# Optimization experiments

Hardware: AMD Instinct MI355X
Metric: run time of the kernel (lower is better)

## Reference

```python
import jax, jax.numpy as jnp
import numpy as np

EPS = 1e-5  # haiku LayerNorm default
BIG = 1e9


def layernorm(x, scale, offset):
    mu = jnp.mean(x, axis=-1, keepdims=True)
    var = jnp.var(x, axis=-1, keepdims=True)
    return scale * (x - mu) * jax.lax.rsqrt(var + EPS) + offset


def setup_inputs() -> dict:
    key = jax.random.key(0)
    ks = iter(jax.random.split(key, 32))
    N_res, N_tok, C, H = 4096, 512, 384, 8
    kd = C // H  # 48, key_dim and value_dim per head
    F = 4 * C    # transition hidden
    s = 0.02
    inp = {
        "original": jax.random.normal(next(ks), (1, N_res, C), jnp.float32),
        "resampled": jax.random.normal(next(ks), (1, N_tok, C), jnp.float32),
        "attention_mask": (jax.random.uniform(next(ks), (H, N_tok, N_res)) < 0.9).astype(jnp.float32),
        "output_mask": jnp.ones((1, N_tok), jnp.float32),
        "input_mask": jnp.ones((1, N_res), jnp.float32),
        # cross-attention LayerNorms
        "qn_scale": jnp.ones((C,), jnp.float32), "qn_offset": jnp.zeros((C,), jnp.float32),
        "dn_scale": jnp.ones((C,), jnp.float32), "dn_offset": jnp.zeros((C,), jnp.float32),
        # attention projections
        "query_w": jax.random.normal(next(ks), (C, H, kd), jnp.float32) * s,
        "key_w": jax.random.normal(next(ks), (C, H, kd), jnp.float32) * s,
        "value_w": jax.random.normal(next(ks), (C, H, kd), jnp.float32) * s,
        "gating_w": jax.random.normal(next(ks), (C, H, kd), jnp.float32) * s,
        "gating_b": jnp.ones((H, kd), jnp.float32),
        "output_w": jax.random.normal(next(ks), (H, kd, C), jnp.float32) * s,
        "output_b": jnp.zeros((C,), jnp.float32),
        # resampled transition
        "rt_ln_scale": jnp.ones((C,), jnp.float32), "rt_ln_offset": jnp.zeros((C,), jnp.float32),
        "rt_w1": jax.random.normal(next(ks), (C, F), jnp.float32) * s, "rt_b1": jnp.zeros((F,), jnp.float32),
        "rt_w2": jax.random.normal(next(ks), (F, C), jnp.float32) * s, "rt_b2": jnp.zeros((C,), jnp.float32),
        # original transition
        "ot_ln_scale": jnp.ones((C,), jnp.float32), "ot_ln_offset": jnp.zeros((C,), jnp.float32),
        "ot_w1": jax.random.normal(next(ks), (C, F), jnp.float32) * s, "ot_b1": jnp.zeros((F,), jnp.float32),
        "ot_w2": jax.random.normal(next(ks), (F, C), jnp.float32) * s, "ot_b2": jnp.zeros((C,), jnp.float32),
    }
    return inp


def reference(original, resampled, attention_mask, output_mask, input_mask,
              qn_scale, qn_offset, dn_scale, dn_offset,
              query_w, key_w, value_w, gating_w, gating_b, output_w, output_b,
              rt_ln_scale, rt_ln_offset, rt_w1, rt_b1, rt_w2, rt_b2,
              ot_ln_scale, ot_ln_offset, ot_w1, ot_b1, ot_w2, ot_b2):
    # ---- CrossAttention (deterministic; dropout rate 0) ----
    bias = BIG * (attention_mask - 1.0)          # [H, T, R]
    q_in = layernorm(resampled, qn_scale, qn_offset)   # [1, T, C]
    d_in = layernorm(original, dn_scale, dn_offset)    # [1, R, C]
    kd = query_w.shape[-1]
    q = jnp.einsum('bqa,ahc->bqhc', q_in, query_w) * kd ** (-0.5)
    k = jnp.einsum('bka,ahc->bkhc', d_in, key_w)
    v = jnp.einsum('bka,ahc->bkhc', d_in, value_w)
    logits = jnp.einsum('bqhc,bkhc->bhqk', q, k) + bias[None]  # [1, H, T, R]
    weights = jax.nn.softmax(logits, axis=-1)
    weighted_avg = jnp.einsum('bhqk,bkhc->bqhc', weights, v)
    gate = jax.nn.sigmoid(jnp.einsum('bqc,chv->bqhv', q_in, gating_w) + gating_b)
    weighted_avg = weighted_avg * gate
    attn_out = jnp.einsum('bqhc,hco->bqo', weighted_avg, output_w) + output_b
    resampled = resampled + attn_out             # residual (dropout off)
    # ---- resampled Transition + residual ----
    t = layernorm(resampled, rt_ln_scale, rt_ln_offset)
    t = jax.nn.relu(t @ rt_w1 + rt_b1) @ rt_w2 + rt_b2
    resampled = resampled + t
    # ---- original Transition + residual ----
    t = layernorm(original, ot_ln_scale, ot_ln_offset)
    t = jax.nn.relu(t @ ot_w1 + ot_b1) @ ot_w2 + ot_b2
    original = original + t
    return resampled.astype(jnp.float32), original.astype(jnp.float32)
```

## Files before the change

kernel.cpp:

```cpp
#include <hip/hip_runtime.h>
#include <hip/hip_bf16.h>
#include <cstdint>

typedef unsigned short u16;
typedef __attribute__((ext_vector_type(8))) __bf16 bf16x8;
typedef __attribute__((ext_vector_type(4))) float f32x4;
typedef __attribute__((ext_vector_type(4))) short s16x4;

#define VSTR 4160

__device__ __forceinline__ u16 f2bf(float f) {
  union { float f; unsigned u; } v; v.f = f;
  unsigned r = (v.u + 0x7FFFu + ((v.u >> 16) & 1u)) >> 16;
  return (u16)r;
}

__device__ __forceinline__ void gll16(const u16* gp, u16* lp) {
  auto g1 = reinterpret_cast<const __attribute__((address_space(1))) void*>(
      reinterpret_cast<uintptr_t>(gp));
  auto l3 = reinterpret_cast<__attribute__((address_space(3))) void*>(
      reinterpret_cast<uintptr_t>(lp));
  __builtin_amdgcn_global_load_lds(g1, l3, 16, 0, 0);
}

__global__ __launch_bounds__(128) void ln_all(
    const float* __restrict__ orig, const float* __restrict__ resam,
    const float* __restrict__ dn_s, const float* __restrict__ dn_o, u16* __restrict__ dinb,
    const float* __restrict__ ot_s, const float* __restrict__ ot_o, u16* __restrict__ otin,
    const float* __restrict__ qn_s, const float* __restrict__ qn_o, u16* __restrict__ qin) {
  const int row = blockIdx.x;
  const int t = threadIdx.x;
  const bool isOrig = row < 4096;
  const float* xr = isOrig ? orig + (size_t)row * 384 : resam + (size_t)(row - 4096) * 384;
  float v0 = xr[t], v1 = xr[t + 128], v2 = xr[t + 256];
  float sum = v0 + v1 + v2;
  float sq = v0 * v0 + v1 * v1 + v2 * v2;
#pragma unroll
  for (int off = 32; off > 0; off >>= 1) {
    sum += __shfl_xor(sum, off);
    sq += __shfl_xor(sq, off);
  }
  __shared__ float red[4];
  if ((t & 63) == 0) { red[(t >> 6) * 2] = sum; red[(t >> 6) * 2 + 1] = sq; }
  __syncthreads();
  sum = red[0] + red[2];
  sq = red[1] + red[3];
  const float mu = sum * (1.f / 384.f);
  const float rstd = rsqrtf(sq * (1.f / 384.f) - mu * mu + 1e-5f);
#pragma unroll
  for (int j = 0; j < 3; ++j) {
    const int cc = t + 128 * j;
    const float xv = (j == 0 ? v0 : (j == 1 ? v1 : v2));
    const float xn = (xv - mu) * rstd;
    if (isOrig) {
      dinb[(size_t)row * 384 + cc] = f2bf(dn_s[cc] * xn + dn_o[cc]);
      otin[(size_t)row * 384 + cc] = f2bf(ot_s[cc] * xn + ot_o[cc]);
    } else {
      qin[(size_t)(row - 4096) * 384 + cc] = f2bf(qn_s[cc] * xn + qn_o[cc]);
    }
  }
}

__global__ __launch_bounds__(128) void ln_kernel(
    const float* __restrict__ x,
    const float* __restrict__ s1, const float* __restrict__ o1, u16* __restrict__ y1) {
  const int row = blockIdx.x;
  const int t = threadIdx.x;
  const float* xr = x + (size_t)row * 384;
  float v0 = xr[t], v1 = xr[t + 128], v2 = xr[t + 256];
  float sum = v0 + v1 + v2;
  float sq = v0 * v0 + v1 * v1 + v2 * v2;
#pragma unroll
  for (int off = 32; off > 0; off >>= 1) {
    sum += __shfl_xor(sum, off);
    sq += __shfl_xor(sq, off);
  }
  __shared__ float red[4];
  if ((t & 63) == 0) { red[(t >> 6) * 2] = sum; red[(t >> 6) * 2 + 1] = sq; }
  __syncthreads();
  sum = red[0] + red[2];
  sq = red[1] + red[3];
  const float mu = sum * (1.f / 384.f);
  const float rstd = rsqrtf(sq * (1.f / 384.f) - mu * mu + 1e-5f);
#pragma unroll
  for (int j = 0; j < 3; ++j) {
    const int cc = t + 128 * j;
    const float xv = (j == 0 ? v0 : (j == 1 ? v1 : v2));
    y1[(size_t)row * 384 + cc] = f2bf(s1[cc] * ((xv - mu) * rstd) + o1[cc]);
  }
}

struct TBatch {
  const float* in[9];
  u16* out[9];
  int K[9], N[9];
  float scale[9];
  int boff[10];
};

__global__ __launch_bounds__(256) void transpose_all(TBatch tb) {
  __shared__ float tile[32][33];
  const int bid = blockIdx.x;
  int j = 0;
  while (j < 8 && bid >= tb.boff[j + 1]) ++j;
  const int lb = bid - tb.boff[j];
  const int NB = tb.N[j] >> 5;
  const int bx = lb % NB, by = lb / NB;
  const float* in = tb.in[j];
  u16* out = tb.out[j];
  const int K = tb.K[j], N = tb.N[j];
  const float scale = tb.scale[j];
  const int tx = threadIdx.x, ty = threadIdx.y;
  const int nb = bx * 32, kb = by * 32;
#pragma unroll
  for (int i = 0; i < 4; ++i)
    tile[ty + 8 * i][tx] = in[(size_t)(kb + ty + 8 * i) * N + nb + tx];
  __syncthreads();
#pragma unroll
  for (int i = 0; i < 4; ++i)
    out[(size_t)(nb + ty + 8 * i) * K + kb + tx] = f2bf(tile[tx][ty + 8 * i] * scale);
}

struct GArgs {
  const u16* A; const u16* Bt;
  int M, N, K, Kld;
  const float* bias; const float* bias2; const float* residual;
  float* outf; u16* outb; u16* outb2;
};

template <int BM, int BN, int EPI>
__global__ __launch_bounds__(256, (BM == 128 ? 2 : 4)) void gemm_bt(GArgs g) {
  constexpr int MT = BM / 32, NT = BN / 32;
  const int tid = threadIdx.x;
  const int w = tid >> 6;
  const int lane = tid & 63;
  const int gq = lane >> 4, c = lane & 15;
  const int brow = blockIdx.y * BM, bcol = blockIdx.x * BN;
  const int wm = (w >> 1) * (BM / 2), wn = (w & 1) * (BN / 2);
  __shared__ u16 As[2][BM][64];
  __shared__ u16 Bs[2][BN][64];
  const int K = g.K;
  const int Kld = g.Kld;
  const size_t koff = (size_t)blockIdx.z * K;

  f32x4 acc[MT][NT];
#pragma unroll
  for (int mt = 0; mt < MT; ++mt)
#pragma unroll
    for (int nt = 0; nt < NT; ++nt)
#pragma unroll
      for (int r = 0; r < 4; ++r) acc[mt][nt][r] = 0.f;

  const int srow = lane >> 3;
  const int schunk = (lane & 7) ^ srow;
  const u16* aSrc = g.A + (size_t)(brow + w * (BM / 4) + srow) * Kld + koff + schunk * 8;
  const u16* bSrc = g.Bt + (size_t)(bcol + w * (BN / 4) + srow) * Kld + koff + schunk * 8;

  auto STAGE = [&](int buf, int k0) {
#pragma unroll
    for (int i = 0; i < BM / 32; ++i)
      gll16(aSrc + (size_t)(8 * i) * Kld + k0, &As[buf][w * (BM / 4) + i * 8][0]);
#pragma unroll
    for (int i = 0; i < BN / 32; ++i)
      gll16(bSrc + (size_t)(8 * i) * Kld + k0, &Bs[buf][w * (BN / 4) + i * 8][0]);
  };

  auto COMPUTE = [&](int buf) {
#pragma unroll
    for (int ks = 0; ks < 2; ++ks) {
      bf16x8 af[MT], bfv[NT];
#pragma unroll
      for (int mt = 0; mt < MT; ++mt) {
        const int row = wm + mt * 16 + c;
        const int ch = ((ks << 2) | gq) ^ (row & 7);
        af[mt] = *(const bf16x8*)&As[buf][row][ch * 8];
      }
#pragma unroll
      for (int nt = 0; nt < NT; ++nt) {
        const int row = wn + nt * 16 + c;
        const int ch = ((ks << 2) | gq) ^ (row & 7);
        bfv[nt] = *(const bf16x8*)&Bs[buf][row][ch * 8];
      }
#pragma unroll
      for (int mt = 0; mt < MT; ++mt)
#pragma unroll
        for (int nt = 0; nt < NT; ++nt)
          acc[mt][nt] =
              __builtin_amdgcn_mfma_f32_16x16x32_bf16(af[mt], bfv[nt], acc[mt][nt], 0, 0, 0);
    }
  };

  const int NTILES = K >> 6;
  STAGE(0, 0);
  __syncthreads();
  int cur = 0;
  for (int t = 0; t < NTILES; ++t) {
    if (t + 1 < NTILES) STAGE(cur ^ 1, (t + 1) << 6);
    COMPUTE(cur);
    __syncthreads();
    cur ^= 1;
  }

  const int N = g.N;
#pragma unroll
  for (int mt = 0; mt < MT; ++mt) {
#pragma unroll
    for (int nt = 0; nt < NT; ++nt) {
      const int n = bcol + wn + nt * 16 + c;
#pragma unroll
      for (int r = 0; r < 4; ++r) {
        const int m = brow + wm + mt * 16 + 4 * gq + r;
        const float v = acc[mt][nt][r];
        if (EPI == 0) {
          g.outb[(size_t)m * N + n] = f2bf(fmaxf(v + g.bias[n], 0.f));
        } else if (EPI == 1) {
          g.outf[(size_t)m * N + n] = v + g.bias[n] + g.residual[(size_t)m * N + n];
        } else if (EPI == 2) {
          if (n < 384)
            g.outb[(size_t)(n / 48) * 4096 * 64 + (size_t)m * 64 + (n % 48)] = f2bf(v);
          else
            g.outb2[(size_t)(n - 384) * VSTR + m] = f2bf(v);
        } else if (EPI == 3) {
          if (n < 384)
            g.outb[(size_t)(n / 48) * 512 * 64 + (size_t)m * 64 + (n % 48)] = f2bf(v);
          else {
            const float sg = v + g.bias2[n - 384];
            g.outf[(size_t)m * 384 + (n - 384)] = 1.f / (1.f + __expf(-sg));
          }
        } else {
          g.outf[(size_t)blockIdx.z * g.M * N + (size_t)m * N + n] = v;
        }
      }
    }
  }
}

struct KIter {
  bf16x8 kA0, kA1, kB0, kB1;
  f32x4 mv0, mv1;
  s16x4 v0, v1, v2, v3, v4, v5;
};

__device__ __forceinline__ KIter load_iter(const u16* __restrict__ khead,
                                           const float* __restrict__ mrow,
                                           const u16* __restrict__ vcol, int rb) {
  KIter I;
  const u16* kr = khead + (size_t)rb * 64;
  I.kA0 = *(const bf16x8*)(kr);
  I.kA1 = *(const bf16x8*)(kr + 32);
  I.kB0 = *(const bf16x8*)(kr + 16 * 64);
  I.kB1 = *(const bf16x8*)(kr + 16 * 64 + 32);
  I.mv0 = *(const f32x4*)(mrow + rb);
  I.mv1 = *(const f32x4*)(mrow + rb + 16);
  const u16* vp0 = vcol + rb;
  I.v0 = *(const s16x4*)(vp0);
  I.v1 = *(const s16x4*)(vp0 + 16);
  const u16* vp1 = vp0 + (size_t)16 * VSTR;
  I.v2 = *(const s16x4*)(vp1);
  I.v3 = *(const s16x4*)(vp1 + 16);
  const u16* vp2 = vp1 + (size_t)16 * VSTR;
  I.v4 = *(const s16x4*)(vp2);
  I.v5 = *(const s16x4*)(vp2 + 16);
  return I;
}

__device__ __forceinline__ void comp_iter(const KIter& I, const bf16x8& qf0,
                                          const bf16x8& qf1, f32x4& O0, f32x4& O1,
                                          f32x4& O2, float& psum) {
  f32x4 z4;
#pragma unroll
  for (int r = 0; r < 4; ++r) z4[r] = 0.f;
  f32x4 s0 = __builtin_amdgcn_mfma_f32_16x16x32_bf16(I.kA0, qf0, z4, 0, 0, 0);
  s0 = __builtin_amdgcn_mfma_f32_16x16x32_bf16(I.kA1, qf1, s0, 0, 0, 0);
  f32x4 s1 = __builtin_amdgcn_mfma_f32_16x16x32_bf16(I.kB0, qf0, z4, 0, 0, 0);
  s1 = __builtin_amdgcn_mfma_f32_16x16x32_bf16(I.kB1, qf1, s1, 0, 0, 0);
  float p0[4], p1[4];
#pragma unroll
  for (int r = 0; r < 4; ++r) {
    p0[r] = I.mv0[r] * __expf(s0[r]);
    p1[r] = I.mv1[r] * __expf(s1[r]);
    psum += p0[r] + p1[r];
  }
  s16x4 pa0, pa1;
  ((unsigned*)&pa0)[0] = __builtin_amdgcn_perm(__builtin_bit_cast(unsigned, p0[1]),
                                               __builtin_bit_cast(unsigned, p0[0]), 0x07060302u);
  ((unsigned*)&pa0)[1] = __builtin_amdgcn_perm(__builtin_bit_cast(unsigned, p0[3]),
                                               __builtin_bit_cast(unsigned, p0[2]), 0x07060302u);
  ((unsigned*)&pa1)[0] = __builtin_amdgcn_perm(__builtin_bit_cast(unsigned, p1[1]),
                                               __builtin_bit_cast(unsigned, p1[0]), 0x07060302u);
  ((unsigned*)&pa1)[1] = __builtin_amdgcn_perm(__builtin_bit_cast(unsigned, p1[3]),
                                               __builtin_bit_cast(unsigned, p1[2]), 0x07060302u);
  O0 = __builtin_amdgcn_mfma_f32_16x16x16bf16_1k(pa0, I.v0, O0, 0, 0, 0);
  O0 = __builtin_amdgcn_mfma_f32_16x16x16bf16_1k(pa1, I.v1, O0, 0, 0, 0);
  O1 = __builtin_amdgcn_mfma_f32_16x16x16bf16_1k(pa0, I.v2, O1, 0, 0, 0);
  O1 = __builtin_amdgcn_mfma_f32_16x16x16bf16_1k(pa1, I.v3, O1, 0, 0, 0);
  O2 = __builtin_amdgcn_mfma_f32_16x16x16bf16_1k(pa0, I.v4, O2, 0, 0, 0);
  O2 = __builtin_amdgcn_mfma_f32_16x16x16bf16_1k(pa1, I.v5, O2, 0, 0, 0);
}

__global__ __launch_bounds__(256, 3) void attn_kernel(
    const u16* __restrict__ Kh, const u16* __restrict__ Qb, const u16* __restrict__ Vt,
    const float* __restrict__ mask, float* __restrict__ partO, float* __restrict__ partL) {
  const int tid = threadIdx.x;
  const int w = tid >> 6;
  const int lane = tid & 63;
  const int gq = lane >> 4, c = lane & 15;
  const int qt = blockIdx.x, h = blockIdx.y, z = blockIdx.z;
  const int tb = qt * 16;
  const int kb = z * 512 + w * 128;

  const u16* qrow = Qb + ((size_t)h * 512 + tb + c) * 64;
  const bf16x8 qf0 = *(const bf16x8*)(qrow + 8 * gq);
  const bf16x8 qf1 = *(const bf16x8*)(qrow + 32 + 8 * gq);

  const u16* khead = Kh + (size_t)h * 4096 * 64 + (size_t)c * 64 + 8 * gq;
  const float* mrow = mask + ((size_t)h * 512 + tb + c) * 4096 + 4 * gq;
  const u16* vcol = Vt + ((size_t)h * 48 + c) * VSTR + 4 * gq;

  f32x4 O0, O1, O2;
#pragma unroll
  for (int r = 0; r < 4; ++r) { O0[r] = 0.f; O1[r] = 0.f; O2[r] = 0.f; }
  float psum = 0.f;

  KIter Ia = load_iter(khead, mrow, vcol, kb);
  KIter Ib = load_iter(khead, mrow, vcol, kb + 32);
  comp_iter(Ia, qf0, qf1, O0, O1, O2, psum);
  Ia = load_iter(khead, mrow, vcol, kb + 64);
  comp_iter(Ib, qf0, qf1, O0, O1, O2, psum);
  Ib = load_iter(khead, mrow, vcol, kb + 96);
  comp_iter(Ia, qf0, qf1, O0, O1, O2, psum);
  comp_iter(Ib, qf0, qf1, O0, O1, O2, psum);

  psum += __shfl_xor(psum, 16);
  psum += __shfl_xor(psum, 32);

  __shared__ float oS[4][16][48];
  __shared__ float lS[4][16];
  if (gq == 0) lS[w][c] = psum;
#pragma unroll
  for (int r = 0; r < 4; ++r) {
    oS[w][4 * gq + r][c] = O0[r];
    oS[w][4 * gq + r][16 + c] = O1[r];
    oS[w][4 * gq + r][32 + c] = O2[r];
  }
  __syncthreads();

  float* pO = partO + (((size_t)z * 32 + qt) * 8 + h) * 768;
  for (int idx = tid; idx < 768; idx += 256) {
    const int q = idx / 48, d = idx % 48;
    float v = 0.f;
#pragma unroll
    for (int ww = 0; ww < 4; ++ww) v += oS[ww][q][d];
    pO[idx] = v;
  }
  if (tid < 16) {
    float L = 0.f;
#pragma unroll
    for (int ww = 0; ww < 4; ++ww) L += lS[ww][tid];
    partL[(((size_t)z * 32 + qt) * 8 + h) * 16 + tid] = L;
  }
}

__global__ __launch_bounds__(256) void attn_merge(
    const float* __restrict__ partO, const float* __restrict__ partL,
    const float* __restrict__ gate, u16* __restrict__ attng) {
  const int qt = blockIdx.x, h = blockIdx.y;
  for (int idx = threadIdx.x; idx < 768; idx += 256) {
    const int q = idx / 48, d = idx % 48;
    float O = 0.f, L = 0.f;
#pragma unroll
    for (int z = 0; z < 8; ++z) {
      O += partO[(((size_t)z * 32 + qt) * 8 + h) * 768 + idx];
      L += partL[(((size_t)z * 32 + qt) * 8 + h) * 16 + q];
    }
    const size_t off = (size_t)(qt * 16 + q) * 384 + h * 48 + d;
    attng[off] = f2bf(O / L * gate[off]);
  }
}

__global__ __launch_bounds__(256) void fmerge(
    const float* __restrict__ pT1, const float* __restrict__ res2,
    const float* __restrict__ rtb2, float* __restrict__ out_res,
    const float* __restrict__ pT2, const float* __restrict__ orig,
    const float* __restrict__ otb2, float* __restrict__ out_orig) {
  const int NT1 = 512 * 384 / 4;
  const int NT2 = 4096 * 384 / 4;
  const int i = blockIdx.x * 256 + threadIdx.x;
  if (i < NT1) {
    const int n0 = (i * 4) % 384;
    f32x4 v = *(const f32x4*)(res2 + (size_t)i * 4);
#pragma unroll
    for (int z = 0; z < 4; ++z) {
      const f32x4 pz = *(const f32x4*)(pT1 + (size_t)z * 512 * 384 + (size_t)i * 4);
#pragma unroll
      for (int r = 0; r < 4; ++r) v[r] += pz[r];
    }
    const f32x4 b = *(const f32x4*)(rtb2 + n0);
#pragma unroll
    for (int r = 0; r < 4; ++r) v[r] += b[r];
    *(f32x4*)(out_res + (size_t)i * 4) = v;
  } else if (i < NT1 + NT2) {
    const int j = i - NT1;
    const int n0 = (j * 4) % 384;
    f32x4 v = *(const f32x4*)(orig + (size_t)j * 4);
#pragma unroll
    for (int z = 0; z < 2; ++z) {
      const f32x4 pz = *(const f32x4*)(pT2 + (size_t)z * 4096 * 384 + (size_t)j * 4);
#pragma unroll
      for (int r = 0; r < 4; ++r) v[r] += pz[r];
    }
    const f32x4 b = *(const f32x4*)(otb2 + n0);
#pragma unroll
    for (int r = 0; r < 4; ++r) v[r] += b[r];
    *(f32x4*)(out_orig + (size_t)j * 4) = v;
  }
}

extern "C" void kernel_launch(void* const* d_in, const int* in_sizes, int n_in,
                              void* d_out, int out_size, void* d_ws, size_t ws_size,
                              hipStream_t stream) {
  (void)in_sizes; (void)n_in; (void)out_size; (void)ws_size;
  const float* original = (const float*)d_in[0];
  const float* resampled = (const float*)d_in[1];
  const float* amask = (const float*)d_in[2];
  const float* qn_s = (const float*)d_in[5];
  const float* qn_o = (const float*)d_in[6];
  const float* dn_s = (const float*)d_in[7];
  const float* dn_o = (const float*)d_in[8];
  const float* w_q = (const float*)d_in[9];
  const float* w_k = (const float*)d_in[10];
  const float* w_v = (const float*)d_in[11];
  const float* w_g = (const float*)d_in[12];
  const float* b_g = (const float*)d_in[13];
  const float* w_o = (const float*)d_in[14];
  const float* b_o = (const float*)d_in[15];
  const float* rt_s = (const float*)d_in[16];
  const float* rt_o = (const float*)d_in[17];
  const float* rtw1 = (const float*)d_in[18];
  const float* rtb1 = (const float*)d_in[19];
  const float* rtw2 = (const float*)d_in[20];
  const float* rtb2 = (const float*)d_in[21];
  const float* ot_s = (const float*)d_in[22];
  const float* ot_o = (const float*)d_in[23];
  const float* otw1 = (const float*)d_in[24];
  const float* otb1 = (const float*)d_in[25];
  const float* otw2 = (const float*)d_in[26];
  const float* otb2 = (const float*)d_in[27];

  float* out_res = (float*)d_out;
  float* out_orig = out_res + 512 * 384;

  char* p = (char*)d_ws;
  auto alloc = [&](size_t n) {
    void* r = (void*)p;
    p += (n + 255) & ~(size_t)255;
    return r;
  };
  u16* Kh = (u16*)alloc((size_t)8 * 4096 * 64 * 2);
  u16* Qb = (u16*)alloc((size_t)8 * 512 * 64 * 2);
  u16* dinb = (u16*)alloc(4096 * 384 * 2);
  u16* otin = (u16*)alloc(4096 * 384 * 2);
  u16* qin = (u16*)alloc(512 * 384 * 2);
  u16* Vt = (u16*)alloc((size_t)384 * VSTR * 2);
  float* gateb = (float*)alloc(512 * 384 * 4);
  u16* attng = (u16*)alloc(512 * 384 * 2);
  float* res2 = (float*)alloc(512 * 384 * 4);
  u16* tin = (u16*)alloc(512 * 384 * 2);
  u16* H1 = (u16*)alloc(512 * 1536 * 2);
  u16* H2 = (u16*)alloc((size_t)4096 * 1536 * 2);
  float* partT1 = (float*)alloc((size_t)4 * 512 * 384 * 4);
  float* partT2 = (float*)alloc((size_t)2 * 4096 * 384 * 4);
  float* partO = partT2;
  float* partL = partT2 + (size_t)8 * 32 * 8 * 768;
  u16* BtKV = (u16*)alloc(768 * 384 * 2);
  u16* BtQG = (u16*)alloc(768 * 384 * 2);
  u16* OwT = (u16*)alloc(384 * 384 * 2);
  u16* Rt1T = (u16*)alloc(1536 * 384 * 2);
  u16* Rt2T = (u16*)alloc(384 * 1536 * 2);
  u16* Ot1T = (u16*)alloc(1536 * 384 * 2);
  u16* Ot2T = (u16*)alloc(384 * 1536 * 2);

  hipMemsetAsync(Kh, 0, (size_t)8 * 4096 * 64 * 2 + (size_t)8 * 512 * 64 * 2, stream);

  {
    TBatch tb{};
    const float qscale = 0.14433756729740643f;
    const float* ins[9] = {w_q, w_g, w_k, w_v, w_o, rtw1, rtw2, otw1, otw2};
    u16* outs[9] = {BtQG, BtQG + 384 * 384, BtKV, BtKV + 384 * 384, OwT,
                    Rt1T, Rt2T, Ot1T, Ot2T};
    const int Ks[9] = {384, 384, 384, 384, 384, 384, 1536, 384, 1536};
    const int Ns[9] = {384, 384, 384, 384, 384, 1536, 384, 1536, 384};
    int off = 0;
    for (int j = 0; j < 9; ++j) {
      tb.in[j] = ins[j]; tb.out[j] = outs[j];
      tb.K[j] = Ks[j]; tb.N[j] = Ns[j];
      tb.scale[j] = (j == 0) ? qscale : 1.f;
      tb.boff[j] = off;
      off += (Ns[j] >> 5) * (Ks[j] >> 5);
    }
    tb.boff[9] = off;
    transpose_all<<<off, dim3(32, 8), 0, stream>>>(tb);
  }

  ln_all<<<4608, 128, 0, stream>>>(original, resampled, dn_s, dn_o, dinb,
                                   ot_s, ot_o, otin, qn_s, qn_o, qin);

  {
    GArgs a{};
    a.A = dinb; a.Bt = BtKV; a.M = 4096; a.N = 768; a.K = 384; a.Kld = 384;
    a.outb = Kh; a.outb2 = Vt;
    gemm_bt<128, 128, 2><<<dim3(6, 32), 256, 0, stream>>>(a);
  }
  {
    GArgs a{};
    a.A = qin; a.Bt = BtQG; a.M = 512; a.N = 768; a.K = 384; a.Kld = 384;
    a.outb = Qb; a.outf = gateb; a.bias2 = b_g;
    gemm_bt<64, 64, 3><<<dim3(12, 8), 256, 0, stream>>>(a);
  }

  attn_kernel<<<dim3(32, 8, 8), 256, 0, stream>>>(Kh, Qb, Vt, amask, partO, partL);
  attn_merge<<<dim3(32, 8), 256, 0, stream>>>(partO, partL, gateb, attng);

  {
    GArgs a{};
    a.A = attng; a.Bt = OwT; a.M = 512; a.N = 384; a.K = 384; a.Kld = 384;
    a.bias = b_o; a.residual = resampled; a.outf = res2;
    gemm_bt<64, 64, 1><<<dim3(6, 8), 256, 0, stream>>>(a);
  }
  ln_kernel<<<512, 128, 0, stream>>>(res2, rt_s, rt_o, tin);
  {
    GArgs a{};
    a.A = tin; a.Bt = Rt1T; a.M = 512; a.N = 1536; a.K = 384; a.Kld = 384;
    a.bias = rtb1; a.outb = H1;
    gemm_bt<64, 64, 0><<<dim3(24, 8), 256, 0, stream>>>(a);
  }
  {
    GArgs a{};
    a.A = H1; a.Bt = Rt2T; a.M = 512; a.N = 384; a.K = 384; a.Kld = 1536;
    a.outf = partT1;
    gemm_bt<64, 64, 4><<<dim3(6, 8, 4), 256, 0, stream>>>(a);
  }
  {
    GArgs a{};
    a.A = otin; a.Bt = Ot1T; a.M = 4096; a.N = 1536; a.K = 384; a.Kld = 384;
    a.bias = otb1; a.outb = H2;
    gemm_bt<128, 128, 0><<<dim3(12, 32), 256, 0, stream>>>(a);
  }
  {
    GArgs a{};
    a.A = H2; a.Bt = Ot2T; a.M = 4096; a.N = 384; a.K = 768; a.Kld = 1536;
    a.outf = partT2;
    gemm_bt<64, 64, 4><<<dim3(6, 64, 2), 256, 0, stream>>>(a);
  }
  fmerge<<<(512 * 384 / 4 + 4096 * 384 / 4 + 255) / 256, 256, 0, stream>>>(
      partT1, res2, rtb2, out_res, partT2, original, otb2, out_orig);
}
```

Measured before the change: 289.1 us.

## Bit-pack attention mask, preload K/V in attention, drop split-K for original transition

A new pre-pass packs the float attention mask into bits, so the attention kernel reads 1 bit per key instead of a 4-byte float. The attention kernel now loads all K and V fragments for its 128-key slice up front into registers behind a schedule barrier, and its occupancy hint is lowered from 3 to 2 blocks. The original-transition second GEMM no longer uses split-K with a separate merge; it fuses bias and residual into its epilogue and writes the output directly, while a smaller merge kernel handles only the resampled path. Costs include an extra mask-packing kernel that still reads the full mask every call, higher register pressure in attention, and half as many blocks for the 4096-row GEMM.

```diff
diff --git a/kernel.cpp b/kernel.cpp
--- a/kernel.cpp
+++ b/kernel.cpp
@@ -6,6 +6,7 @@
 typedef __attribute__((ext_vector_type(8))) __bf16 bf16x8;
 typedef __attribute__((ext_vector_type(4))) float f32x4;
 typedef __attribute__((ext_vector_type(4))) short s16x4;
+typedef __attribute__((ext_vector_type(4))) unsigned u32x4;
 
 #define VSTR 4160
 
@@ -21,6 +22,20 @@
   auto l3 = reinterpret_cast<__attribute__((address_space(3))) void*>(
       reinterpret_cast<uintptr_t>(lp));
   __builtin_amdgcn_global_load_lds(g1, l3, 16, 0, 0);
+}
+
+__global__ __launch_bounds__(256) void mask_bits(const float* __restrict__ mask,
+                                                 u16* __restrict__ mb) {
+  const int t = blockIdx.x * 256 + threadIdx.x;
+  const float* src = mask + (size_t)t * 16;
+  unsigned b = 0;
+#pragma unroll
+  for (int j = 0; j < 4; ++j) {
+    const f32x4 v = *(const f32x4*)(src + 4 * j);
+#pragma unroll
+    for (int k = 0; k < 4; ++k) b |= (v[k] != 0.f ? 1u : 0u) << (4 * j + k);
+  }
+  mb[t] = (u16)b;
 }
 
 __global__ __launch_bounds__(128) void ln_all(
@@ -235,72 +250,10 @@
   }
 }
 
-struct KIter {
-  bf16x8 kA0, kA1, kB0, kB1;
-  f32x4 mv0, mv1;
-  s16x4 v0, v1, v2, v3, v4, v5;
-};
-
-__device__ __forceinline__ KIter load_iter(const u16* __restrict__ khead,
-                                           const float* __restrict__ mrow,
-                                           const u16* __restrict__ vcol, int rb) {
-  KIter I;
-  const u16* kr = khead + (size_t)rb * 64;
-  I.kA0 = *(const bf16x8*)(kr);
-  I.kA1 = *(const bf16x8*)(kr + 32);
-  I.kB0 = *(const bf16x8*)(kr + 16 * 64);
-  I.kB1 = *(const bf16x8*)(kr + 16 * 64 + 32);
-  I.mv0 = *(const f32x4*)(mrow + rb);
-  I.mv1 = *(const f32x4*)(mrow + rb + 16);
-  const u16* vp0 = vcol + rb;
-  I.v0 = *(const s16x4*)(vp0);
-  I.v1 = *(const s16x4*)(vp0 + 16);
-  const u16* vp1 = vp0 + (size_t)16 * VSTR;
-  I.v2 = *(const s16x4*)(vp1);
-  I.v3 = *(const s16x4*)(vp1 + 16);
-  const u16* vp2 = vp1 + (size_t)16 * VSTR;
-  I.v4 = *(const s16x4*)(vp2);
-  I.v5 = *(const s16x4*)(vp2 + 16);
-  return I;
-}
-
-__device__ __forceinline__ void comp_iter(const KIter& I, const bf16x8& qf0,
-                                          const bf16x8& qf1, f32x4& O0, f32x4& O1,
-                                          f32x4& O2, float& psum) {
-  f32x4 z4;
-#pragma unroll
-  for (int r = 0; r < 4; ++r) z4[r] = 0.f;
-  f32x4 s0 = __builtin_amdgcn_mfma_f32_16x16x32_bf16(I.kA0, qf0, z4, 0, 0, 0);
-  s0 = __builtin_amdgcn_mfma_f32_16x16x32_bf16(I.kA1, qf1, s0, 0, 0, 0);
-  f32x4 s1 = __builtin_amdgcn_mfma_f32_16x16x32_bf16(I.kB0, qf0, z4, 0, 0, 0);
-  s1 = __builtin_amdgcn_mfma_f32_16x16x32_bf16(I.kB1, qf1, s1, 0, 0, 0);
-  float p0[4], p1[4];
-#pragma unroll
-  for (int r = 0; r < 4; ++r) {
-    p0[r] = I.mv0[r] * __expf(s0[r]);
-    p1[r] = I.mv1[r] * __expf(s1[r]);
-    psum += p0[r] + p1[r];
-  }
-  s16x4 pa0, pa1;
-  ((unsigned*)&pa0)[0] = __builtin_amdgcn_perm(__builtin_bit_cast(unsigned, p0[1]),
-                                               __builtin_bit_cast(unsigned, p0[0]), 0x07060302u);
-  ((unsigned*)&pa0)[1] = __builtin_amdgcn_perm(__builtin_bit_cast(unsigned, p0[3]),
-                                               __builtin_bit_cast(unsigned, p0[2]), 0x07060302u);
-  ((unsigned*)&pa1)[0] = __builtin_amdgcn_perm(__builtin_bit_cast(unsigned, p1[1]),
-                                               __builtin_bit_cast(unsigned, p1[0]), 0x07060302u);
-  ((unsigned*)&pa1)[1] = __builtin_amdgcn_perm(__builtin_bit_cast(unsigned, p1[3]),
-                                               __builtin_bit_cast(unsigned, p1[2]), 0x07060302u);
-  O0 = __builtin_amdgcn_mfma_f32_16x16x16bf16_1k(pa0, I.v0, O0, 0, 0, 0);
-  O0 = __builtin_amdgcn_mfma_f32_16x16x16bf16_1k(pa1, I.v1, O0, 0, 0, 0);
-  O1 = __builtin_amdgcn_mfma_f32_16x16x16bf16_1k(pa0, I.v2, O1, 0, 0, 0);
-  O1 = __builtin_amdgcn_mfma_f32_16x16x16bf16_1k(pa1, I.v3, O1, 0, 0, 0);
-  O2 = __builtin_amdgcn_mfma_f32_16x16x16bf16_1k(pa0, I.v4, O2, 0, 0, 0);
-  O2 = __builtin_amdgcn_mfma_f32_16x16x16bf16_1k(pa1, I.v5, O2, 0, 0, 0);
-}
-
-__global__ __launch_bounds__(256, 3) void attn_kernel(
+__global__ __launch_bounds__(256, 2) void attn_kernel(
     const u16* __restrict__ Kh, const u16* __restrict__ Qb, const u16* __restrict__ Vt,
-    const float* __restrict__ mask, float* __restrict__ partO, float* __restrict__ partL) {
+    const unsigned char* __restrict__ mbits, float* __restrict__ partO,
+    float* __restrict__ partL) {
   const int tid = threadIdx.x;
   const int w = tid >> 6;
   const int lane = tid & 63;
@@ -313,23 +266,73 @@
   const bf16x8 qf0 = *(const bf16x8*)(qrow + 8 * gq);
   const bf16x8 qf1 = *(const bf16x8*)(qrow + 32 + 8 * gq);
 
-  const u16* khead = Kh + (size_t)h * 4096 * 64 + (size_t)c * 64 + 8 * gq;
-  const float* mrow = mask + ((size_t)h * 512 + tb + c) * 4096 + 4 * gq;
-  const u16* vcol = Vt + ((size_t)h * 48 + c) * VSTR + 4 * gq;
+  const u16* kbase = Kh + (size_t)h * 4096 * 64 + (size_t)(kb + c) * 64 + 8 * gq;
+  bf16x8 kf[16];
+#pragma unroll
+  for (int it = 0; it < 4; ++it) {
+    const u16* kr = kbase + it * 32 * 64;
+    kf[4 * it + 0] = *(const bf16x8*)(kr);
+    kf[4 * it + 1] = *(const bf16x8*)(kr + 32);
+    kf[4 * it + 2] = *(const bf16x8*)(kr + 16 * 64);
+    kf[4 * it + 3] = *(const bf16x8*)(kr + 16 * 64 + 32);
+  }
+
+  s16x4 vv[4][3][2];
+#pragma unroll
+  for (int nt = 0; nt < 3; ++nt) {
+    const u16* vc = Vt + ((size_t)h * 48 + nt * 16 + c) * VSTR + kb + 4 * gq;
+#pragma unroll
+    for (int it = 0; it < 4; ++it) {
+      vv[it][nt][0] = *(const s16x4*)(vc + it * 32);
+      vv[it][nt][1] = *(const s16x4*)(vc + it * 32 + 16);
+    }
+  }
+
+  const u32x4 mb =
+      *(const u32x4*)(mbits + ((size_t)h * 512 + tb + c) * 512 + (kb >> 3));
+
+  __builtin_amdgcn_sched_barrier(0);
 
   f32x4 O0, O1, O2;
 #pragma unroll
   for (int r = 0; r < 4; ++r) { O0[r] = 0.f; O1[r] = 0.f; O2[r] = 0.f; }
   float psum = 0.f;
 
-  KIter Ia = load_iter(khead, mrow, vcol, kb);
-  KIter Ib = load_iter(khead, mrow, vcol, kb + 32);
-  comp_iter(Ia, qf0, qf1, O0, O1, O2, psum);
-  Ia = load_iter(khead, mrow, vcol, kb + 64);
-  comp_iter(Ib, qf0, qf1, O0, O1, O2, psum);
-  Ib = load_iter(khead, mrow, vcol, kb + 96);
-  comp_iter(Ia, qf0, qf1, O0, O1, O2, psum);
-  comp_iter(Ib, qf0, qf1, O0, O1, O2, psum);
+#pragma unroll
+  for (int it = 0; it < 4; ++it) {
+    f32x4 z4;
+#pragma unroll
+    for (int r = 0; r < 4; ++r) z4[r] = 0.f;
+    f32x4 s0 = __builtin_amdgcn_mfma_f32_16x16x32_bf16(kf[4 * it + 0], qf0, z4, 0, 0, 0);
+    s0 = __builtin_amdgcn_mfma_f32_16x16x32_bf16(kf[4 * it + 1], qf1, s0, 0, 0, 0);
+    f32x4 s1 = __builtin_amdgcn_mfma_f32_16x16x32_bf16(kf[4 * it + 2], qf0, z4, 0, 0, 0);
+    s1 = __builtin_amdgcn_mfma_f32_16x16x32_bf16(kf[4 * it + 3], qf1, s1, 0, 0, 0);
+
+    const unsigned wd0 = mb[it] >> (4 * gq);
+    const unsigned wd1 = mb[it] >> (16 + 4 * gq);
+    float p0[4], p1[4];
+#pragma unroll
+    for (int r = 0; r < 4; ++r) {
+      p0[r] = ((wd0 >> r) & 1u) ? __expf(s0[r]) : 0.f;
+      p1[r] = ((wd1 >> r) & 1u) ? __expf(s1[r]) : 0.f;
+      psum += p0[r] + p1[r];
+    }
+    s16x4 pa0, pa1;
+    ((unsigned*)&pa0)[0] = __builtin_amdgcn_perm(__builtin_bit_cast(unsigned, p0[1]),
+                                                 __builtin_bit_cast(unsigned, p0[0]), 0x07060302u);
+    ((unsigned*)&pa0)[1] = __builtin_amdgcn_perm(__builtin_bit_cast(unsigned, p0[3]),
+                                                 __builtin_bit_cast(unsigned, p0[2]), 0x07060302u);
+    ((unsigned*)&pa1)[0] = __builtin_amdgcn_perm(__builtin_bit_cast(unsigned, p1[1]),
+                                                 __builtin_bit_cast(unsigned, p1[0]), 0x07060302u);
+    ((unsigned*)&pa1)[1] = __builtin_amdgcn_perm(__builtin_bit_cast(unsigned, p1[3]),
+                                                 __builtin_bit_cast(unsigned, p1[2]), 0x07060302u);
+    O0 = __builtin_amdgcn_mfma_f32_16x16x16bf16_1k(pa0, vv[it][0][0], O0, 0, 0, 0);
+    O0 = __builtin_amdgcn_mfma_f32_16x16x16bf16_1k(pa1, vv[it][0][1], O0, 0, 0, 0);
+    O1 = __builtin_amdgcn_mfma_f32_16x16x16bf16_1k(pa0, vv[it][1][0], O1, 0, 0, 0);
+    O1 = __builtin_amdgcn_mfma_f32_16x16x16bf16_1k(pa1, vv[it][1][1], O1, 0, 0, 0);
+    O2 = __builtin_amdgcn_mfma_f32_16x16x16bf16_1k(pa0, vv[it][2][0], O2, 0, 0, 0);
+    O2 = __builtin_amdgcn_mfma_f32_16x16x16bf16_1k(pa1, vv[it][2][1], O2, 0, 0, 0);
+  }
 
   psum += __shfl_xor(psum, 16);
   psum += __shfl_xor(psum, 32);
@@ -378,42 +381,22 @@
   }
 }
 
-__global__ __launch_bounds__(256) void fmerge(
+__global__ __launch_bounds__(256) void merge_res(
     const float* __restrict__ pT1, const float* __restrict__ res2,
-    const float* __restrict__ rtb2, float* __restrict__ out_res,
-    const float* __restrict__ pT2, const float* __restrict__ orig,
-    const float* __restrict__ otb2, float* __restrict__ out_orig) {
-  const int NT1 = 512 * 384 / 4;
-  const int NT2 = 4096 * 384 / 4;
+    const float* __restrict__ rtb2, float* __restrict__ out_res) {
   const int i = blockIdx.x * 256 + threadIdx.x;
-  if (i < NT1) {
-    const int n0 = (i * 4) % 384;
-    f32x4 v = *(const f32x4*)(res2 + (size_t)i * 4);
-#pragma unroll
-    for (int z = 0; z < 4; ++z) {
-      const f32x4 pz = *(const f32x4*)(pT1 + (size_t)z * 512 * 384 + (size_t)i * 4);
-#pragma unroll
-      for (int r = 0; r < 4; ++r) v[r] += pz[r];
-    }
-    const f32x4 b = *(const f32x4*)(rtb2 + n0);
-#pragma unroll
-    for (int r = 0; r < 4; ++r) v[r] += b[r];
-    *(f32x4*)(out_res + (size_t)i * 4) = v;
-  } else if (i < NT1 + NT2) {
-    const int j = i - NT1;
-    const int n0 = (j * 4) % 384;
-    f32x4 v = *(const f32x4*)(orig + (size_t)j * 4);
-#pragma unroll
-    for (int z = 0; z < 2; ++z) {
-      const f32x4 pz = *(const f32x4*)(pT2 + (size_t)z * 4096 * 384 + (size_t)j * 4);
-#pragma unroll
-      for (int r = 0; r < 4; ++r) v[r] += pz[r];
-    }
-    const f32x4 b = *(const f32x4*)(otb2 + n0);
-#pragma unroll
-    for (int r = 0; r < 4; ++r) v[r] += b[r];
-    *(f32x4*)(out_orig + (size_t)j * 4) = v;
-  }
+  const int n0 = (i * 4) % 384;
+  f32x4 v = *(const f32x4*)(res2 + (size_t)i * 4);
+#pragma unroll
+  for (int z = 0; z < 4; ++z) {
+    const f32x4 pz = *(const f32x4*)(pT1 + (size_t)z * 512 * 384 + (size_t)i * 4);
+#pragma unroll
+    for (int r = 0; r < 4; ++r) v[r] += pz[r];
+  }
+  const f32x4 b = *(const f32x4*)(rtb2 + n0);
+#pragma unroll
+  for (int r = 0; r < 4; ++r) v[r] += b[r];
+  *(f32x4*)(out_res + (size_t)i * 4) = v;
 }
 
 extern "C" void kernel_launch(void* const* d_in, const int* in_sizes, int n_in,
@@ -469,9 +452,9 @@
   u16* H1 = (u16*)alloc(512 * 1536 * 2);
   u16* H2 = (u16*)alloc((size_t)4096 * 1536 * 2);
   float* partT1 = (float*)alloc((size_t)4 * 512 * 384 * 4);
-  float* partT2 = (float*)alloc((size_t)2 * 4096 * 384 * 4);
-  float* partO = partT2;
-  float* partL = partT2 + (size_t)8 * 32 * 8 * 768;
+  float* partO = (float*)alloc((size_t)8 * 32 * 8 * 768 * 4);
+  float* partL = (float*)alloc((size_t)8 * 32 * 8 * 16 * 4);
+  u16* mbitsB = (u16*)alloc((size_t)8 * 512 * 512);
   u16* BtKV = (u16*)alloc(768 * 384 * 2);
   u16* BtQG = (u16*)alloc(768 * 384 * 2);
   u16* OwT = (u16*)alloc(384 * 384 * 2);
@@ -481,6 +464,8 @@
   u16* Ot2T = (u16*)alloc(384 * 1536 * 2);
 
   hipMemsetAsync(Kh, 0, (size_t)8 * 4096 * 64 * 2 + (size_t)8 * 512 * 64 * 2, stream);
+
+  mask_bits<<<4096, 256, 0, stream>>>(amask, mbitsB);
 
   {
     TBatch tb{};
@@ -518,7 +503,8 @@
     gemm_bt<64, 64, 3><<<dim3(12, 8), 256, 0, stream>>>(a);
   }
 
-  attn_kernel<<<dim3(32, 8, 8), 256, 0, stream>>>(Kh, Qb, Vt, amask, partO, partL);
+  attn_kernel<<<dim3(32, 8, 8), 256, 0, stream>>>(
+      Kh, Qb, Vt, (const unsigned char*)mbitsB, partO, partL);
   attn_merge<<<dim3(32, 8), 256, 0, stream>>>(partO, partL, gateb, attng);
 
   {
@@ -548,10 +534,9 @@
   }
   {
     GArgs a{};
-    a.A = H2; a.Bt = Ot2T; a.M = 4096; a.N = 384; a.K = 768; a.Kld = 1536;
-    a.outf = partT2;
-    gemm_bt<64, 64, 4><<<dim3(6, 64, 2), 256, 0, stream>>>(a);
-  }
-  fmerge<<<(512 * 384 / 4 + 4096 * 384 / 4 + 255) / 256, 256, 0, stream>>>(
-      partT1, res2, rtb2, out_res, partT2, original, otb2, out_orig);
-}
+    a.A = H2; a.Bt = Ot2T; a.M = 4096; a.N = 384; a.K = 1536; a.Kld = 1536;
+    a.bias = otb2; a.residual = original; a.outf = out_orig;
+    gemm_bt<64, 64, 1><<<dim3(6, 64), 256, 0, stream>>>(a);
+  }
+  merge_res<<<192, 256, 0, stream>>>(partT1, res2, rtb2, out_res);
+}
```

After: 291.7 us. Within noise of the previous version (+0.9%).
